# Performance work log

Measured on AMD Instinct MI355X. Metric: run time of the kernel, lower is better.

The kernel has to match this reference:

```python
import jax, jax.numpy as jnp
import numpy as np

N = 50000    # nodes
E = 600000   # edges
D = 128      # emb_dim
L = 5        # num_layer
VA = 64      # atom feature vocab (per column)
VB = 8       # bond feature vocab (per column)
BN_EPS = 1e-5


def setup_inputs() -> dict:
    key = jax.random.key(0)
    ks = jax.random.split(key, 10)
    x = jax.random.randint(ks[0], (N, 9), 0, VA)
    edge_index = jax.random.randint(ks[1], (2, E), 0, N)
    edge_attr = jax.random.randint(ks[2], (E, 3), 0, VB)
    edge_weight = jax.random.uniform(ks[3], (E,), dtype=jnp.float32)
    s = 0.05
    atom_emb = jax.random.normal(ks[4], (9, VA, D), dtype=jnp.float32) * s
    bond_emb = jax.random.normal(ks[5], (L, 3, VB, D), dtype=jnp.float32) * s
    W1 = jax.random.normal(ks[6], (L, D, 2 * D), dtype=jnp.float32) / np.sqrt(D)
    b1 = jnp.zeros((L, 2 * D), jnp.float32)
    bn1_g = jnp.ones((L, 2 * D), jnp.float32)
    bn1_b = jnp.zeros((L, 2 * D), jnp.float32)
    W2 = jax.random.normal(ks[7], (L, 2 * D, D), dtype=jnp.float32) / np.sqrt(2 * D)
    b2 = jnp.zeros((L, D), jnp.float32)
    eps_p = jnp.zeros((L,), jnp.float32)       # GIN eps per layer
    bn_g = jnp.ones((L, D), jnp.float32)       # outer BatchNorm per layer
    bn_b = jnp.zeros((L, D), jnp.float32)
    return dict(x=x, edge_index=edge_index, edge_attr=edge_attr, edge_weight=edge_weight,
                atom_emb=atom_emb, bond_emb=bond_emb, W1=W1, b1=b1, bn1_g=bn1_g,
                bn1_b=bn1_b, W2=W2, b2=b2, eps_p=eps_p, bn_g=bn_g, bn_b=bn_b)


def _bn(z, g, b):
    # training-mode batch norm over the node dimension
    m = z.mean(axis=0)
    v = z.var(axis=0)
    return (z - m) * jax.lax.rsqrt(v + BN_EPS) * g + b


def reference(x, edge_index, edge_attr, edge_weight, atom_emb, bond_emb,
              W1, b1, bn1_g, bn1_b, W2, b2, eps_p, bn_g, bn_b):
    src, dst = edge_index[0], edge_index[1]
    ew = edge_weight[:, None]                                  # [E,1]
    # AtomEncoder: sum of per-column embedding lookups -> [N,D]
    h = sum(atom_emb[f][x[:, f]] for f in range(9))
    for l in range(L):
        # BondEncoder -> [E,D]
        ea = sum(bond_emb[l, f][edge_attr[:, f]] for f in range(3))
        # message: relu(x_j + edge_emb) * edge_weight, scatter-add to dst
        msg = jax.nn.relu(h[src] + ea) * ew                    # [E,D]
        agg = jax.ops.segment_sum(msg, dst, num_segments=N)    # [N,D]
        z = (1.0 + eps_p[l]) * h + agg
        # GIN MLP: Linear -> BN -> ReLU -> Linear
        z = jax.nn.relu(_bn(z @ W1[l] + b1[l], bn1_g[l], bn1_b[l]))
        z = z @ W2[l] + b2[l]
        # outer BatchNorm, ReLU except last layer (dropout is identity at p=0)
        z = _bn(z, bn_g[l], bn_b[l])
        if l < L - 1:
            z = jax.nn.relu(z)
        h = z
    return h  # JK == 'last'
```

## Files before the change

kernel.cpp:

```cpp
#include <hip/hip_runtime.h>

#define NN 50000
#define EE 600000
#define DD 128
#define DD2 256
#define LL 5
#define BN_EPS 1e-5f
#define GXF 512
#define NT1 782
#define SPAD 16

typedef __attribute__((ext_vector_type(8))) _Float16 half8;
typedef __attribute__((ext_vector_type(4))) float f32x4;

__device__ inline unsigned short f2h_bits(float f) {
    _Float16 h = (_Float16)f;
    return __builtin_bit_cast(unsigned short, h);
}
__device__ inline float h2f(unsigned short u) {
    return (float)__builtin_bit_cast(_Float16, u);
}
__device__ inline half8 bnrelu8(half8 v, half8 s, half8 t) {
    half8 r = v * s + t;
#pragma unroll
    for (int k = 0; k < 8; k++) r[k] = (r[k] > (_Float16)0) ? r[k] : (_Float16)0;
    return r;
}


__device__ inline void grid_barrier(int* bar) {
    asm volatile("s_waitcnt vmcnt(0)" ::: "memory");
    __syncthreads();
    if (threadIdx.x == 0) {
        int g = blockIdx.x & 7;
        bool done = false;
        int t = __hip_atomic_fetch_add(&bar[g * 16], 1, __ATOMIC_RELAXED,
                                       __HIP_MEMORY_SCOPE_AGENT);
        if (t == (GXF / 8) - 1) {
            int m = __hip_atomic_fetch_add(&bar[128], 1, __ATOMIC_RELAXED,
                                           __HIP_MEMORY_SCOPE_AGENT);
            if (m == 7) {
                __hip_atomic_store(&bar[144], 1, __ATOMIC_RELAXED, __HIP_MEMORY_SCOPE_AGENT);
                done = true;
            }
        }
        if (!done) {
            while (__hip_atomic_load(&bar[144], __ATOMIC_RELAXED, __HIP_MEMORY_SCOPE_AGENT) == 0)
                __builtin_amdgcn_s_sleep(8);
        }
    }
    __syncthreads();
}


__global__ void hist_kernel(const int* __restrict__ dst, int* __restrict__ counts) {
    int e = blockIdx.x * blockDim.x + threadIdx.x;
    if (e < EE) atomicAdd(&counts[dst[e]], 1);
}

__global__ void scan1_kernel(const int* __restrict__ counts, int* __restrict__ row_ptr,
                             int* __restrict__ blksum) {
    __shared__ int tmp[256];
    int i = blockIdx.x * 256 + threadIdx.x;
    int v = (i < NN) ? counts[i] : 0;
    tmp[threadIdx.x] = v;
    __syncthreads();
    for (int off = 1; off < 256; off <<= 1) {
        int x = 0;
        if (threadIdx.x >= off) x = tmp[threadIdx.x - off];
        __syncthreads();
        if (threadIdx.x >= off) tmp[threadIdx.x] += x;
        __syncthreads();
    }
    if (i < NN) row_ptr[i] = tmp[threadIdx.x] - v;
    if (threadIdx.x == 255) blksum[blockIdx.x] = tmp[255];
}

__global__ void scan2_kernel(int* __restrict__ blksum, int nblocks) {
    __shared__ int tmp[256];
    int v = (threadIdx.x < nblocks) ? blksum[threadIdx.x] : 0;
    tmp[threadIdx.x] = v;
    __syncthreads();
    for (int off = 1; off < 256; off <<= 1) {
        int x = 0;
        if (threadIdx.x >= off) x = tmp[threadIdx.x - off];
        __syncthreads();
        if (threadIdx.x >= off) tmp[threadIdx.x] += x;
        __syncthreads();
    }
    blksum[threadIdx.x] = tmp[threadIdx.x] - v;
}

__global__ void scan3_kernel(int* __restrict__ row_ptr, const int* __restrict__ blksum) {
    int i = blockIdx.x * 256 + threadIdx.x;
    if (i < NN) row_ptr[i] += blksum[blockIdx.x];
    if (i == 0) row_ptr[NN] = EE;
}

__global__ void scatter_kernel(const int* __restrict__ dst, const int* __restrict__ src,
                               const int* __restrict__ edge_attr, const float* __restrict__ ew,
                               const int* __restrict__ row_ptr, int* __restrict__ cursor,
                               uint2* __restrict__ edata) {
    int e = blockIdx.x * blockDim.x + threadIdx.x;
    if (e < EE) {
        int d = dst[e];
        int p = row_ptr[d] + atomicAdd(&cursor[d], 1);
        int cid = edge_attr[3 * e + 0] + 8 * edge_attr[3 * e + 1] + 64 * edge_attr[3 * e + 2];
        uint2 v;
        v.x = (unsigned)src[e];
        v.y = (unsigned)cid | ((unsigned)f2h_bits(ew[e]) << 16);
        edata[p] = v;
    }
}


__global__ void prep_tables_kernel(const float* __restrict__ W1, const float* __restrict__ W2,
                                   const float* __restrict__ bond_emb,
                                   unsigned short* __restrict__ W1t,
                                   unsigned short* __restrict__ W2t,
                                   unsigned short* __restrict__ bsum) {
    const int NW = LL * DD * DD2;
    int idx = blockIdx.x * 256 + threadIdx.x;
    if (idx < NW) {
        int l = idx / (DD * DD2);
        int rem = idx - l * DD * DD2;
        int k = rem / DD2, m = rem - k * DD2;
        W1t[(size_t)l * DD * DD2 + (size_t)m * DD + k] = f2h_bits(W1[idx]);
    } else if (idx < 2 * NW) {
        int j = idx - NW;
        int l = j / (DD * DD2);
        int rem = j - l * DD * DD2;
        int k = rem / DD, m = rem - k * DD;
        W2t[(size_t)l * DD * DD2 + (size_t)m * DD2 + k] = f2h_bits(W2[j]);
    } else if (idx < 2 * NW + LL * 512 * DD) {
        int j = idx - 2 * NW;
        int l = j >> 16;
        int rem = j & 65535;
        int cid = rem >> 7, d = rem & 127;
        int a0 = cid & 7, a1 = (cid >> 3) & 7, a2 = cid >> 6;
        const float* base = bond_emb + (size_t)l * 3 * 8 * DD;
        bsum[j] = f2h_bits(base[a0 * DD + d] + base[(8 + a1) * DD + d] + base[(16 + a2) * DD + d]);
    }
}


__global__ void init_h_kernel(const int* __restrict__ x, const float* __restrict__ atom_emb,
                              unsigned short* __restrict__ h) {
    int n = blockIdx.x * 8 + (threadIdx.x >> 5);
    int lane = threadIdx.x & 31;
    float a0 = 0.f, a1 = 0.f, a2 = 0.f, a3 = 0.f;
#pragma unroll
    for (int f = 0; f < 9; f++) {
        int idx = x[n * 9 + f];
        const float4 v = *(const float4*)(atom_emb + ((size_t)(f * 64 + idx) * DD) + lane * 4);
        a0 += v.x; a1 += v.y; a2 += v.z; a3 += v.w;
    }
    ushort4 o;
    o.x = f2h_bits(a0); o.y = f2h_bits(a1); o.z = f2h_bits(a2); o.w = f2h_bits(a3);
    *(ushort4*)(h + (size_t)n * DD + lane * 4) = o;
}


template <bool FUSE>
__global__ void agg_kernel(const unsigned short* __restrict__ hsrc,
                           const float* __restrict__ stats, const float* __restrict__ g,
                           const float* __restrict__ bb, const int* __restrict__ row_ptr,
                           const uint2* __restrict__ edata,
                           const unsigned short* __restrict__ bsum_l,
                           const float* __restrict__ eps_ptr, unsigned short* __restrict__ Aout) {
    int n = blockIdx.x * 8 + (threadIdx.x >> 5);
    int lane = threadIdx.x & 31;
    int c0 = lane * 4;

    float bs[4] = {1.f, 1.f, 1.f, 1.f}, bt[4] = {0.f, 0.f, 0.f, 0.f};
    if (FUSE) {
        float4 gg = *(const float4*)(g + c0);
        float4 bv = *(const float4*)(bb + c0);
        float gv[4] = {gg.x, gg.y, gg.z, gg.w};
        float bbv[4] = {bv.x, bv.y, bv.z, bv.w};
#pragma unroll
        for (int k = 0; k < 4; k++) {
            float sm = stats[(size_t)(512 + c0 + k) * SPAD];
            float sq = stats[(size_t)(640 + c0 + k) * SPAD];
            float mean = sm * (1.f / NN);
            float var = sq * (1.f / NN) - mean * mean;
            bs[k] = gv[k] * rsqrtf(var + BN_EPS);
            bt[k] = bbv[k] - mean * bs[k];
        }
    }

    auto accum = [&](uint2 ed, uint2 hz, uint2 bz, float* acc) {
        float w = h2f((unsigned short)(ed.y >> 16));
        unsigned int hw[2] = {hz.x, hz.y}, bw[2] = {bz.x, bz.y};
#pragma unroll
        for (int k = 0; k < 2; k++) {
            float hv0 = h2f((unsigned short)(hw[k] & 0xffff));
            float hv1 = h2f((unsigned short)(hw[k] >> 16));
            if (FUSE) {
                hv0 = fmaxf(hv0 * bs[2 * k] + bt[2 * k], 0.f);
                hv1 = fmaxf(hv1 * bs[2 * k + 1] + bt[2 * k + 1], 0.f);
            }
            float m0 = fmaxf(hv0 + h2f((unsigned short)(bw[k] & 0xffff)), 0.f);
            float m1 = fmaxf(hv1 + h2f((unsigned short)(bw[k] >> 16)), 0.f);
            acc[2 * k] += m0 * w;
            acc[2 * k + 1] += m1 * w;
        }
    };

    int beg = row_ptr[n], end = row_ptr[n + 1];
    float acc[4] = {0.f, 0.f, 0.f, 0.f};
    int i = beg;
    for (; i + 4 <= end; i += 4) {
        uint2 e0 = edata[i], e1 = edata[i + 1], e2 = edata[i + 2], e3 = edata[i + 3];
        uint2 h0 = *(const uint2*)(hsrc + (size_t)e0.x * DD + c0);
        uint2 b0 = *(const uint2*)(bsum_l + (size_t)(e0.y & 0xffff) * DD + c0);
        uint2 h1 = *(const uint2*)(hsrc + (size_t)e1.x * DD + c0);
        uint2 b1 = *(const uint2*)(bsum_l + (size_t)(e1.y & 0xffff) * DD + c0);
        uint2 h2 = *(const uint2*)(hsrc + (size_t)e2.x * DD + c0);
        uint2 b2 = *(const uint2*)(bsum_l + (size_t)(e2.y & 0xffff) * DD + c0);
        uint2 h3 = *(const uint2*)(hsrc + (size_t)e3.x * DD + c0);
        uint2 b3 = *(const uint2*)(bsum_l + (size_t)(e3.y & 0xffff) * DD + c0);
        accum(e0, h0, b0, acc);
        accum(e1, h1, b1, acc);
        accum(e2, h2, b2, acc);
        accum(e3, h3, b3, acc);
    }
    for (; i < end; i++) {
        uint2 e0 = edata[i];
        uint2 h0 = *(const uint2*)(hsrc + (size_t)e0.x * DD + c0);
        uint2 b0 = *(const uint2*)(bsum_l + (size_t)(e0.y & 0xffff) * DD + c0);
        accum(e0, h0, b0, acc);
    }

    float eps1 = 1.f + eps_ptr[0];
    uint2 hz = *(const uint2*)(hsrc + (size_t)n * DD + c0);
    unsigned int hw[2] = {hz.x, hz.y};
    float self[4];
#pragma unroll
    for (int k = 0; k < 2; k++) {
        float hv0 = h2f((unsigned short)(hw[k] & 0xffff));
        float hv1 = h2f((unsigned short)(hw[k] >> 16));
        if (FUSE) {
            hv0 = fmaxf(hv0 * bs[2 * k] + bt[2 * k], 0.f);
            hv1 = fmaxf(hv1 * bs[2 * k + 1] + bt[2 * k + 1], 0.f);
        }
        self[2 * k] = hv0;
        self[2 * k + 1] = hv1;
    }
    ushort4 o;
    o.x = f2h_bits(eps1 * self[0] + acc[0]);
    o.y = f2h_bits(eps1 * self[1] + acc[1]);
    o.z = f2h_bits(eps1 * self[2] + acc[2]);
    o.w = f2h_bits(eps1 * self[3] + acc[3]);
    *(ushort4*)(Aout + (size_t)n * DD + c0) = o;
}


__global__ __launch_bounds__(256, 2) void fused_mlp_kernel(
    const unsigned short* __restrict__ A, const unsigned short* __restrict__ W1,
    const float* __restrict__ b1, const unsigned short* __restrict__ W2,
    const float* __restrict__ b2, const float* __restrict__ g1,
    const float* __restrict__ bb1, unsigned short* __restrict__ z2,
    float* __restrict__ statsL, int* bar) {
    __shared__ __align__(16) char ldsb[65536];
    __shared__ __align__(16) float st_sh[2 * DD2];
    const int lane = threadIdx.x & 63;
    const int wave = threadIdx.x >> 6;
    const int lr = lane & 15;
    const int q = lane >> 4;
    const int swz = (lr & 7) << 4;

    {
        const int wcol = wave * 64;
        half8 wf[4][4];
#pragma unroll
        for (int jm = 0; jm < 4; jm++) {
            const unsigned short* p = W1 + (size_t)(wcol + jm * 16 + lr) * DD + q * 8;
#pragma unroll
            for (int ks = 0; ks < 4; ks++)
                wf[jm][ks] = __builtin_bit_cast(half8, *(const int4*)(p + ks * 32));
        }
        float bi[4][4];
#pragma unroll
        for (int jm = 0; jm < 4; jm++)
#pragma unroll
            for (int r = 0; r < 4; r++) bi[jm][r] = b1[wcol + jm * 16 + q * 4 + r];

        float s1[16], sq1[16];
#pragma unroll
        for (int k = 0; k < 16; k++) { s1[k] = 0.f; sq1[k] = 0.f; }

        for (int s = 0; s < 2; s++) {
            int t = blockIdx.x + s * GXF;
            if (t >= NT1) break;
            int row0 = t * 64;
            const unsigned short* ap0 = A + (size_t)(row0 + lr) * DD + q * 8;
            f32x4 acc[4][4];
#pragma unroll
            for (int jm = 0; jm < 4; jm++)
#pragma unroll
                for (int in = 0; in < 4; in++) acc[jm][in] = (f32x4){0.f, 0.f, 0.f, 0.f};
#pragma unroll
            for (int ks = 0; ks < 4; ks++) {
                half8 rf[4];
#pragma unroll
                for (int in = 0; in < 4; in++)
                    rf[in] = __builtin_bit_cast(
                        half8, *(const int4*)(ap0 + (size_t)(in * 16) * DD + ks * 32));
#pragma unroll
                for (int jm = 0; jm < 4; jm++)
#pragma unroll
                    for (int in = 0; in < 4; in++)
                        acc[jm][in] = __builtin_amdgcn_mfma_f32_16x16x32_f16(
                            wf[jm][ks], rf[in], acc[jm][in], 0, 0, 0);
            }
            char* slot = ldsb + s * 32768;
#pragma unroll
            for (int in = 0; in < 4; in++) {
                int row = in * 16 + lr;
                bool rv = (row0 + row) < NN;
                int rbase = row * 512 + wave * 128;
#pragma unroll
                for (int jm = 0; jm < 4; jm++) {
                    ushort4 o;
#pragma unroll
                    for (int r = 0; r < 4; r++) {
                        float v = acc[jm][in][r] + bi[jm][r];
                        ((unsigned short*)&o)[r] = f2h_bits(v);
                        if (rv) {
                            s1[jm * 4 + r] += v;
                            sq1[jm * 4 + r] += v * v;
                        }
                    }
                    *(ushort4*)(slot + ((rbase + jm * 32 + q * 8) ^ swz)) = o;
                }
            }
        }
#pragma unroll
        for (int k = 0; k < 16; k++) {
            float a = s1[k], b = sq1[k];
#pragma unroll
            for (int m = 1; m < 16; m <<= 1) {
                a += __shfl_xor(a, m);
                b += __shfl_xor(b, m);
            }
            if (lr == 0) {
                int c = wcol + (k >> 2) * 16 + q * 4 + (k & 3);
                unsafeAtomicAdd(&statsL[(size_t)c * SPAD], a);
                unsafeAtomicAdd(&statsL[(size_t)(DD2 + c) * SPAD], b);
            }
        }
    }

    grid_barrier(bar);

    {
        for (int c = threadIdx.x; c < DD2; c += 256) {
            float sv = __hip_atomic_load(&statsL[(size_t)c * SPAD], __ATOMIC_RELAXED,
                                         __HIP_MEMORY_SCOPE_AGENT);
            float qv = __hip_atomic_load(&statsL[(size_t)(DD2 + c) * SPAD], __ATOMIC_RELAXED,
                                         __HIP_MEMORY_SCOPE_AGENT);
            float mean = sv * (1.f / NN);
            float var = qv * (1.f / NN) - mean * mean;
            float sc = g1[c] * rsqrtf(var + BN_EPS);
            st_sh[c] = sc;
            st_sh[DD2 + c] = bb1[c] - mean * sc;
        }
        __syncthreads();

        const int cb2 = wave * 32;
        half8 sa[8], ta[8];
#pragma unroll
        for (int ks = 0; ks < 8; ks++) {
            const float* sp = st_sh + ks * 32 + q * 8;
            float4 sA = *(const float4*)(sp);
            float4 sB = *(const float4*)(sp + 4);
            float4 tA = *(const float4*)(sp + DD2);
            float4 tB = *(const float4*)(sp + DD2 + 4);
            sa[ks] = (half8){(_Float16)sA.x, (_Float16)sA.y, (_Float16)sA.z, (_Float16)sA.w,
                             (_Float16)sB.x, (_Float16)sB.y, (_Float16)sB.z, (_Float16)sB.w};
            ta[ks] = (half8){(_Float16)tA.x, (_Float16)tA.y, (_Float16)tA.z, (_Float16)tA.w,
                             (_Float16)tB.x, (_Float16)tB.y, (_Float16)tB.z, (_Float16)tB.w};
        }
        half8 wf2[2][8];
#pragma unroll
        for (int jm = 0; jm < 2; jm++) {
            const unsigned short* p = W2 + (size_t)(cb2 + jm * 16 + lr) * DD2 + q * 8;
#pragma unroll
            for (int ks = 0; ks < 8; ks++)
                wf2[jm][ks] = __builtin_bit_cast(half8, *(const int4*)(p + ks * 32));
        }
        float bi2[2][4];
#pragma unroll
        for (int jm = 0; jm < 2; jm++)
#pragma unroll
            for (int r = 0; r < 4; r++) bi2[jm][r] = b2[cb2 + jm * 16 + q * 4 + r];

        float s2[8], sq2[8];
#pragma unroll
        for (int k = 0; k < 8; k++) { s2[k] = 0.f; sq2[k] = 0.f; }

        for (int s = 0; s < 2; s++) {
            int t = blockIdx.x + s * GXF;
            if (t >= NT1) break;
            int row0 = t * 64;
            char* slot = ldsb + s * 32768;
            f32x4 acc[2][4];
#pragma unroll
            for (int jm = 0; jm < 2; jm++)
#pragma unroll
                for (int in = 0; in < 4; in++) acc[jm][in] = (f32x4){0.f, 0.f, 0.f, 0.f};
#pragma unroll
            for (int ks = 0; ks < 8; ks++) {
                half8 rf[4];
#pragma unroll
                for (int in = 0; in < 4; in++) {
                    int row = in * 16 + lr;
                    half8 z = *(const half8*)(slot + ((row * 512 + ks * 64 + q * 16) ^ swz));
                    rf[in] = bnrelu8(z, sa[ks], ta[ks]);
                }
#pragma unroll
                for (int jm = 0; jm < 2; jm++)
#pragma unroll
                    for (int in = 0; in < 4; in++)
                        acc[jm][in] = __builtin_amdgcn_mfma_f32_16x16x32_f16(
                            wf2[jm][ks], rf[in], acc[jm][in], 0, 0, 0);
            }
#pragma unroll
            for (int in = 0; in < 4; in++) {
                int row = row0 + in * 16 + lr;
                if (row < NN) {
#pragma unroll
                    for (int jm = 0; jm < 2; jm++) {
                        ushort4 o;
#pragma unroll
                        for (int r = 0; r < 4; r++) {
                            float v = acc[jm][in][r] + bi2[jm][r];
                            ((unsigned short*)&o)[r] = f2h_bits(v);
                            s2[jm * 4 + r] += v;
                            sq2[jm * 4 + r] += v * v;
                        }
                        *(ushort4*)(z2 + (size_t)row * DD + cb2 + jm * 16 + q * 4) = o;
                    }
                }
            }
        }
#pragma unroll
        for (int k = 0; k < 8; k++) {
            float a = s2[k], b = sq2[k];
#pragma unroll
            for (int m = 1; m < 16; m <<= 1) {
                a += __shfl_xor(a, m);
                b += __shfl_xor(b, m);
            }
            if (lr == 0) {
                int c = cb2 + (k >> 2) * 16 + q * 4 + (k & 3);
                unsafeAtomicAdd(&statsL[(size_t)(512 + c) * SPAD], a);
                unsafeAtomicAdd(&statsL[(size_t)(640 + c) * SPAD], b);
            }
        }
    }
}


__global__ void bnapply2_last_kernel(const unsigned short* __restrict__ z,
                                     const float* __restrict__ stats, const float* __restrict__ g,
                                     const float* __restrict__ bb, float* __restrict__ fout) {
    __shared__ float s_sh[DD], t_sh[DD];
    if (threadIdx.x < DD) {
        int c = threadIdx.x;
        float mean = stats[(size_t)(512 + c) * SPAD] * (1.f / NN);
        float var = stats[(size_t)(640 + c) * SPAD] * (1.f / NN) - mean * mean;
        float sc = g[c] * rsqrtf(var + BN_EPS);
        s_sh[c] = sc;
        t_sh[c] = bb[c] - mean * sc;
    }
    __syncthreads();
    int i = (blockIdx.x * 256 + threadIdx.x) * 4;
    int c = i & 127;
    uint2 in = *(const uint2*)(z + i);
    float4 out;
    out.x = h2f((unsigned short)(in.x & 0xffff)) * s_sh[c] + t_sh[c];
    out.y = h2f((unsigned short)(in.x >> 16)) * s_sh[c + 1] + t_sh[c + 1];
    out.z = h2f((unsigned short)(in.y & 0xffff)) * s_sh[c + 2] + t_sh[c + 2];
    out.w = h2f((unsigned short)(in.y >> 16)) * s_sh[c + 3] + t_sh[c + 3];
    *(float4*)(fout + i) = out;
}


extern "C" void kernel_launch(void* const* d_in, const int* in_sizes, int n_in,
                              void* d_out, int out_size, void* d_ws, size_t ws_size,
                              hipStream_t stream) {
    const int* x = (const int*)d_in[0];
    const int* edge_index = (const int*)d_in[1];
    const int* edge_attr = (const int*)d_in[2];
    const float* edge_weight = (const float*)d_in[3];
    const float* atom_emb = (const float*)d_in[4];
    const float* bond_emb = (const float*)d_in[5];
    const float* W1 = (const float*)d_in[6];
    const float* b1 = (const float*)d_in[7];
    const float* bn1_g = (const float*)d_in[8];
    const float* bn1_b = (const float*)d_in[9];
    const float* W2 = (const float*)d_in[10];
    const float* b2 = (const float*)d_in[11];
    const float* eps_p = (const float*)d_in[12];
    const float* bn_g = (const float*)d_in[13];
    const float* bn_b = (const float*)d_in[14];
    const int* srcv = edge_index;
    const int* dstv = edge_index + EE;

    char* p = (char*)d_ws;
    auto alloc = [&](size_t bytes) {
        void* r = (void*)p;
        p += (bytes + 255) & ~(size_t)255;
        return r;
    };
    unsigned short* h = (unsigned short*)alloc((size_t)NN * DD * 2);
    unsigned short* A1h = (unsigned short*)alloc((size_t)(NT1 * 64) * DD * 2);
    unsigned short* z2 = (unsigned short*)alloc((size_t)NN * DD * 2);
    uint2* edata = (uint2*)alloc((size_t)EE * 8);
    int* counts = (int*)alloc((size_t)NN * 4);
    int* row_ptr = (int*)alloc((size_t)(NN + 1) * 4);
    int* blksum = (int*)alloc(256 * 4);
    unsigned short* W1t = (unsigned short*)alloc((size_t)LL * DD * DD2 * 2);
    unsigned short* W2t = (unsigned short*)alloc((size_t)LL * DD * DD2 * 2);
    unsigned short* bsum = (unsigned short*)alloc((size_t)LL * 512 * DD * 2);
    const size_t statsFloats = (size_t)LL * 768 * SPAD;
    const size_t barInts = (size_t)LL * 160;
    float* statsP = (float*)alloc(statsFloats * 4 + barInts * 4);
    int* barBase = (int*)(statsP + statsFloats);

    hipMemsetAsync(counts, 0, (size_t)NN * 4, stream);
    hipMemsetAsync(statsP, 0, statsFloats * 4 + barInts * 4, stream);
    hist_kernel<<<(EE + 255) / 256, 256, 0, stream>>>(dstv, counts);
    int nblk = (NN + 255) / 256;
    scan1_kernel<<<nblk, 256, 0, stream>>>(counts, row_ptr, blksum);
    scan2_kernel<<<1, 256, 0, stream>>>(blksum, nblk);
    scan3_kernel<<<nblk, 256, 0, stream>>>(row_ptr, blksum);
    hipMemsetAsync(counts, 0, (size_t)NN * 4, stream);
    scatter_kernel<<<(EE + 255) / 256, 256, 0, stream>>>(dstv, srcv, edge_attr, edge_weight,
                                                         row_ptr, counts, edata);
    prep_tables_kernel<<<(2 * LL * DD * DD2 + LL * 512 * DD + 255) / 256, 256, 0, stream>>>(
        W1, W2, bond_emb, W1t, W2t, bsum);
    init_h_kernel<<<NN / 8, 256, 0, stream>>>(x, atom_emb, h);

    for (int l = 0; l < LL; l++) {
        float* statsL = statsP + (size_t)l * 768 * SPAD;
        const unsigned short* bsum_l = bsum + (size_t)l * 512 * DD;

        if (l == 0) {
            agg_kernel<false><<<NN / 8, 256, 0, stream>>>(h, nullptr, nullptr, nullptr, row_ptr,
                                                          edata, bsum_l, eps_p + l, A1h);
        } else {
            agg_kernel<true><<<NN / 8, 256, 0, stream>>>(
                z2, statsP + (size_t)(l - 1) * 768 * SPAD, bn_g + (l - 1) * DD,
                bn_b + (l - 1) * DD, row_ptr, edata, bsum_l, eps_p + l, A1h);
        }

        fused_mlp_kernel<<<GXF, 256, 0, stream>>>(
            A1h, W1t + (size_t)l * DD * DD2, b1 + l * DD2, W2t + (size_t)l * DD * DD2,
            b2 + l * DD, bn1_g + l * DD2, bn1_b + l * DD2, z2, statsL, barBase + l * 160);
    }

    bnapply2_last_kernel<<<NN * DD / 1024, 256, 0, stream>>>(
        z2, statsP + (size_t)(LL - 1) * 768 * SPAD, bn_g + (LL - 1) * DD, bn_b + (LL - 1) * DD,
        (float*)d_out);
}
```

Measured before the change: 791.5 us.

## Split fused persistent MLP kernel into two GEMM kernels via global intermediate

Replaces the persistent fused MLP kernel, which used a software grid barrier and kept the first-layer output in LDS, with two separate kernels. The first GEMM now writes a 256-wide fp16 intermediate to global memory and the second reads it back. This removes the spin-wait barrier and the 64KB LDS buffer per block, which may let more blocks run and avoids barrier stalls. The cost is an extra kernel launch per layer and roughly 50MB of extra global traffic per layer.

```diff
diff --git a/kernel.cpp b/kernel.cpp
--- a/kernel.cpp
+++ b/kernel.cpp
@@ -6,7 +6,6 @@
 #define DD2 256
 #define LL 5
 #define BN_EPS 1e-5f
-#define GXF 512
 #define NT1 782
 #define SPAD 16
 
@@ -27,30 +26,6 @@
     return r;
 }
 
-
-__device__ inline void grid_barrier(int* bar) {
-    asm volatile("s_waitcnt vmcnt(0)" ::: "memory");
-    __syncthreads();
-    if (threadIdx.x == 0) {
-        int g = blockIdx.x & 7;
-        bool done = false;
-        int t = __hip_atomic_fetch_add(&bar[g * 16], 1, __ATOMIC_RELAXED,
-                                       __HIP_MEMORY_SCOPE_AGENT);
-        if (t == (GXF / 8) - 1) {
-            int m = __hip_atomic_fetch_add(&bar[128], 1, __ATOMIC_RELAXED,
-                                           __HIP_MEMORY_SCOPE_AGENT);
-            if (m == 7) {
-                __hip_atomic_store(&bar[144], 1, __ATOMIC_RELAXED, __HIP_MEMORY_SCOPE_AGENT);
-                done = true;
-            }
-        }
-        if (!done) {
-            while (__hip_atomic_load(&bar[144], __ATOMIC_RELAXED, __HIP_MEMORY_SCOPE_AGENT) == 0)
-                __builtin_amdgcn_s_sleep(8);
-        }
-    }
-    __syncthreads();
-}
 
 
 __global__ void hist_kernel(const int* __restrict__ dst, int* __restrict__ counts) {
@@ -256,208 +231,198 @@
 }
 
 
-__global__ __launch_bounds__(256, 2) void fused_mlp_kernel(
-    const unsigned short* __restrict__ A, const unsigned short* __restrict__ W1,
-    const float* __restrict__ b1, const unsigned short* __restrict__ W2,
-    const float* __restrict__ b2, const float* __restrict__ g1,
-    const float* __restrict__ bb1, unsigned short* __restrict__ z2,
-    float* __restrict__ statsL, int* bar) {
-    __shared__ __align__(16) char ldsb[65536];
+__global__ __launch_bounds__(256, 2) void gemm1_kernel(const unsigned short* __restrict__ A,
+                                                       const unsigned short* __restrict__ W1,
+                                                       const float* __restrict__ b1,
+                                                       unsigned short* __restrict__ z1,
+                                                       float* __restrict__ statsL) {
+    const int lane = threadIdx.x & 63;
+    const int wave = threadIdx.x >> 6;
+    const int lr = lane & 15;
+    const int q = lane >> 4;
+    const int wcol = wave * 64;
+
+    half8 wf[4][4];
+#pragma unroll
+    for (int jm = 0; jm < 4; jm++) {
+        const unsigned short* p = W1 + (size_t)(wcol + jm * 16 + lr) * DD + q * 8;
+#pragma unroll
+        for (int ks = 0; ks < 4; ks++)
+            wf[jm][ks] = __builtin_bit_cast(half8, *(const int4*)(p + ks * 32));
+    }
+    float bi[4][4];
+#pragma unroll
+    for (int jm = 0; jm < 4; jm++)
+#pragma unroll
+        for (int r = 0; r < 4; r++) bi[jm][r] = b1[wcol + jm * 16 + q * 4 + r];
+
+    int row0 = blockIdx.x * 64;
+    const unsigned short* ap0 = A + (size_t)(row0 + lr) * DD + q * 8;
+    f32x4 acc[4][4];
+#pragma unroll
+    for (int jm = 0; jm < 4; jm++)
+#pragma unroll
+        for (int in = 0; in < 4; in++) acc[jm][in] = (f32x4){0.f, 0.f, 0.f, 0.f};
+#pragma unroll
+    for (int ks = 0; ks < 4; ks++) {
+        half8 rf[4];
+#pragma unroll
+        for (int in = 0; in < 4; in++)
+            rf[in] =
+                __builtin_bit_cast(half8, *(const int4*)(ap0 + (size_t)(in * 16) * DD + ks * 32));
+#pragma unroll
+        for (int jm = 0; jm < 4; jm++)
+#pragma unroll
+            for (int in = 0; in < 4; in++)
+                acc[jm][in] =
+                    __builtin_amdgcn_mfma_f32_16x16x32_f16(wf[jm][ks], rf[in], acc[jm][in], 0, 0, 0);
+    }
+
+    float s1[16], sq1[16];
+#pragma unroll
+    for (int k = 0; k < 16; k++) { s1[k] = 0.f; sq1[k] = 0.f; }
+#pragma unroll
+    for (int in = 0; in < 4; in++) {
+        int row = row0 + in * 16 + lr;
+        bool rv = row < NN;
+#pragma unroll
+        for (int jm = 0; jm < 4; jm++) {
+            ushort4 o;
+#pragma unroll
+            for (int r = 0; r < 4; r++) {
+                float v = acc[jm][in][r] + bi[jm][r];
+                ((unsigned short*)&o)[r] = f2h_bits(v);
+                if (rv) {
+                    s1[jm * 4 + r] += v;
+                    sq1[jm * 4 + r] += v * v;
+                }
+            }
+            if (rv) *(ushort4*)(z1 + (size_t)row * DD2 + wcol + jm * 16 + q * 4) = o;
+        }
+    }
+#pragma unroll
+    for (int k = 0; k < 16; k++) {
+        float a = s1[k], b = sq1[k];
+#pragma unroll
+        for (int m = 1; m < 16; m <<= 1) {
+            a += __shfl_xor(a, m);
+            b += __shfl_xor(b, m);
+        }
+        if (lr == 0) {
+            int c = wcol + (k >> 2) * 16 + q * 4 + (k & 3);
+            unsafeAtomicAdd(&statsL[(size_t)c * SPAD], a);
+            unsafeAtomicAdd(&statsL[(size_t)(DD2 + c) * SPAD], b);
+        }
+    }
+}
+
+
+__global__ __launch_bounds__(256, 2) void gemm2_kernel(
+    const unsigned short* __restrict__ z1, const unsigned short* __restrict__ W2,
+    const float* __restrict__ b2, const float* __restrict__ g1, const float* __restrict__ bb1,
+    unsigned short* __restrict__ z2, float* __restrict__ statsL) {
     __shared__ __align__(16) float st_sh[2 * DD2];
     const int lane = threadIdx.x & 63;
     const int wave = threadIdx.x >> 6;
     const int lr = lane & 15;
     const int q = lane >> 4;
-    const int swz = (lr & 7) << 4;
 
     {
-        const int wcol = wave * 64;
-        half8 wf[4][4];
-#pragma unroll
-        for (int jm = 0; jm < 4; jm++) {
-            const unsigned short* p = W1 + (size_t)(wcol + jm * 16 + lr) * DD + q * 8;
-#pragma unroll
-            for (int ks = 0; ks < 4; ks++)
-                wf[jm][ks] = __builtin_bit_cast(half8, *(const int4*)(p + ks * 32));
-        }
-        float bi[4][4];
-#pragma unroll
-        for (int jm = 0; jm < 4; jm++)
-#pragma unroll
-            for (int r = 0; r < 4; r++) bi[jm][r] = b1[wcol + jm * 16 + q * 4 + r];
-
-        float s1[16], sq1[16];
-#pragma unroll
-        for (int k = 0; k < 16; k++) { s1[k] = 0.f; sq1[k] = 0.f; }
-
-        for (int s = 0; s < 2; s++) {
-            int t = blockIdx.x + s * GXF;
-            if (t >= NT1) break;
-            int row0 = t * 64;
-            const unsigned short* ap0 = A + (size_t)(row0 + lr) * DD + q * 8;
-            f32x4 acc[4][4];
-#pragma unroll
-            for (int jm = 0; jm < 4; jm++)
-#pragma unroll
-                for (int in = 0; in < 4; in++) acc[jm][in] = (f32x4){0.f, 0.f, 0.f, 0.f};
-#pragma unroll
-            for (int ks = 0; ks < 4; ks++) {
-                half8 rf[4];
-#pragma unroll
-                for (int in = 0; in < 4; in++)
-                    rf[in] = __builtin_bit_cast(
-                        half8, *(const int4*)(ap0 + (size_t)(in * 16) * DD + ks * 32));
-#pragma unroll
-                for (int jm = 0; jm < 4; jm++)
-#pragma unroll
-                    for (int in = 0; in < 4; in++)
-                        acc[jm][in] = __builtin_amdgcn_mfma_f32_16x16x32_f16(
-                            wf[jm][ks], rf[in], acc[jm][in], 0, 0, 0);
+        int c = threadIdx.x;
+        float sv = statsL[(size_t)c * SPAD];
+        float qv = statsL[(size_t)(DD2 + c) * SPAD];
+        float mean = sv * (1.f / NN);
+        float var = qv * (1.f / NN) - mean * mean;
+        float sc = g1[c] * rsqrtf(var + BN_EPS);
+        st_sh[c] = sc;
+        st_sh[DD2 + c] = bb1[c] - mean * sc;
+    }
+    __syncthreads();
+
+    const int cb2 = wave * 32;
+    half8 sa[8], ta[8];
+#pragma unroll
+    for (int ks = 0; ks < 8; ks++) {
+        const float* sp = st_sh + ks * 32 + q * 8;
+        float4 sA = *(const float4*)(sp);
+        float4 sB = *(const float4*)(sp + 4);
+        float4 tA = *(const float4*)(sp + DD2);
+        float4 tB = *(const float4*)(sp + DD2 + 4);
+        sa[ks] = (half8){(_Float16)sA.x, (_Float16)sA.y, (_Float16)sA.z, (_Float16)sA.w,
+                         (_Float16)sB.x, (_Float16)sB.y, (_Float16)sB.z, (_Float16)sB.w};
+        ta[ks] = (half8){(_Float16)tA.x, (_Float16)tA.y, (_Float16)tA.z, (_Float16)tA.w,
+                         (_Float16)tB.x, (_Float16)tB.y, (_Float16)tB.z, (_Float16)tB.w};
+    }
+    half8 wf2[2][8];
+#pragma unroll
+    for (int jm = 0; jm < 2; jm++) {
+        const unsigned short* p = W2 + (size_t)(cb2 + jm * 16 + lr) * DD2 + q * 8;
+#pragma unroll
+        for (int ks = 0; ks < 8; ks++)
+            wf2[jm][ks] = __builtin_bit_cast(half8, *(const int4*)(p + ks * 32));
+    }
+    float bi2[2][4];
+#pragma unroll
+    for (int jm = 0; jm < 2; jm++)
+#pragma unroll
+        for (int r = 0; r < 4; r++) bi2[jm][r] = b2[cb2 + jm * 16 + q * 4 + r];
+
+    int row0 = blockIdx.x * 64;
+    f32x4 acc[2][4];
+#pragma unroll
+    for (int jm = 0; jm < 2; jm++)
+#pragma unroll
+        for (int in = 0; in < 4; in++) acc[jm][in] = (f32x4){0.f, 0.f, 0.f, 0.f};
+#pragma unroll
+    for (int ks = 0; ks < 8; ks++) {
+        half8 rf[4];
+#pragma unroll
+        for (int in = 0; in < 4; in++) {
+            int row = row0 + in * 16 + lr;
+            half8 z = *(const half8*)(z1 + (size_t)row * DD2 + ks * 32 + q * 8);
+            rf[in] = bnrelu8(z, sa[ks], ta[ks]);
+        }
+#pragma unroll
+        for (int jm = 0; jm < 2; jm++)
+#pragma unroll
+            for (int in = 0; in < 4; in++)
+                acc[jm][in] = __builtin_amdgcn_mfma_f32_16x16x32_f16(wf2[jm][ks], rf[in],
+                                                                     acc[jm][in], 0, 0, 0);
+    }
+
+    float s2[8], sq2[8];
+#pragma unroll
+    for (int k = 0; k < 8; k++) { s2[k] = 0.f; sq2[k] = 0.f; }
+#pragma unroll
+    for (int in = 0; in < 4; in++) {
+        int row = row0 + in * 16 + lr;
+        if (row < NN) {
+#pragma unroll
+            for (int jm = 0; jm < 2; jm++) {
+                ushort4 o;
+#pragma unroll
+                for (int r = 0; r < 4; r++) {
+                    float v = acc[jm][in][r] + bi2[jm][r];
+                    ((unsigned short*)&o)[r] = f2h_bits(v);
+                    s2[jm * 4 + r] += v;
+                    sq2[jm * 4 + r] += v * v;
+                }
+                *(ushort4*)(z2 + (size_t)row * DD + cb2 + jm * 16 + q * 4) = o;
             }
-            char* slot = ldsb + s * 32768;
-#pragma unroll
-            for (int in = 0; in < 4; in++) {
-                int row = in * 16 + lr;
-                bool rv = (row0 + row) < NN;
-                int rbase = row * 512 + wave * 128;
-#pragma unroll
-                for (int jm = 0; jm < 4; jm++) {
-                    ushort4 o;
-#pragma unroll
-                    for (int r = 0; r < 4; r++) {
-                        float v = acc[jm][in][r] + bi[jm][r];
-                        ((unsigned short*)&o)[r] = f2h_bits(v);
-                        if (rv) {
-                            s1[jm * 4 + r] += v;
-                            sq1[jm * 4 + r] += v * v;
-                        }
-                    }
-                    *(ushort4*)(slot + ((rbase + jm * 32 + q * 8) ^ swz)) = o;
-                }
-            }
-        }
-#pragma unroll
-        for (int k = 0; k < 16; k++) {
-            float a = s1[k], b = sq1[k];
-#pragma unroll
-            for (int m = 1; m < 16; m <<= 1) {
-                a += __shfl_xor(a, m);
-                b += __shfl_xor(b, m);
-            }
-            if (lr == 0) {
-                int c = wcol + (k >> 2) * 16 + q * 4 + (k & 3);
-                unsafeAtomicAdd(&statsL[(size_t)c * SPAD], a);
-                unsafeAtomicAdd(&statsL[(size_t)(DD2 + c) * SPAD], b);
-            }
-        }
-    }
-
-    grid_barrier(bar);
-
-    {
-        for (int c = threadIdx.x; c < DD2; c += 256) {
-            float sv = __hip_atomic_load(&statsL[(size_t)c * SPAD], __ATOMIC_RELAXED,
-                                         __HIP_MEMORY_SCOPE_AGENT);
-            float qv = __hip_atomic_load(&statsL[(size_t)(DD2 + c) * SPAD], __ATOMIC_RELAXED,
-                                         __HIP_MEMORY_SCOPE_AGENT);
-            float mean = sv * (1.f / NN);
-            float var = qv * (1.f / NN) - mean * mean;
-            float sc = g1[c] * rsqrtf(var + BN_EPS);
-            st_sh[c] = sc;
-            st_sh[DD2 + c] = bb1[c] - mean * sc;
-        }
-        __syncthreads();
-
-        const int cb2 = wave * 32;
-        half8 sa[8], ta[8];
-#pragma unroll
-        for (int ks = 0; ks < 8; ks++) {
-            const float* sp = st_sh + ks * 32 + q * 8;
-            float4 sA = *(const float4*)(sp);
-            float4 sB = *(const float4*)(sp + 4);
-            float4 tA = *(const float4*)(sp + DD2);
-            float4 tB = *(const float4*)(sp + DD2 + 4);
-            sa[ks] = (half8){(_Float16)sA.x, (_Float16)sA.y, (_Float16)sA.z, (_Float16)sA.w,
-                             (_Float16)sB.x, (_Float16)sB.y, (_Float16)sB.z, (_Float16)sB.w};
-            ta[ks] = (half8){(_Float16)tA.x, (_Float16)tA.y, (_Float16)tA.z, (_Float16)tA.w,
-                             (_Float16)tB.x, (_Float16)tB.y, (_Float16)tB.z, (_Float16)tB.w};
-        }
-        half8 wf2[2][8];
-#pragma unroll
-        for (int jm = 0; jm < 2; jm++) {
-            const unsigned short* p = W2 + (size_t)(cb2 + jm * 16 + lr) * DD2 + q * 8;
-#pragma unroll
-            for (int ks = 0; ks < 8; ks++)
-                wf2[jm][ks] = __builtin_bit_cast(half8, *(const int4*)(p + ks * 32));
-        }
-        float bi2[2][4];
-#pragma unroll
-        for (int jm = 0; jm < 2; jm++)
-#pragma unroll
-            for (int r = 0; r < 4; r++) bi2[jm][r] = b2[cb2 + jm * 16 + q * 4 + r];
-
-        float s2[8], sq2[8];
-#pragma unroll
-        for (int k = 0; k < 8; k++) { s2[k] = 0.f; sq2[k] = 0.f; }
-
-        for (int s = 0; s < 2; s++) {
-            int t = blockIdx.x + s * GXF;
-            if (t >= NT1) break;
-            int row0 = t * 64;
-            char* slot = ldsb + s * 32768;
-            f32x4 acc[2][4];
-#pragma unroll
-            for (int jm = 0; jm < 2; jm++)
-#pragma unroll
-                for (int in = 0; in < 4; in++) acc[jm][in] = (f32x4){0.f, 0.f, 0.f, 0.f};
-#pragma unroll
-            for (int ks = 0; ks < 8; ks++) {
-                half8 rf[4];
-#pragma unroll
-                for (int in = 0; in < 4; in++) {
-                    int row = in * 16 + lr;
-                    half8 z = *(const half8*)(slot + ((row * 512 + ks * 64 + q * 16) ^ swz));
-                    rf[in] = bnrelu8(z, sa[ks], ta[ks]);
-                }
-#pragma unroll
-                for (int jm = 0; jm < 2; jm++)
-#pragma unroll
-                    for (int in = 0; in < 4; in++)
-                        acc[jm][in] = __builtin_amdgcn_mfma_f32_16x16x32_f16(
-                            wf2[jm][ks], rf[in], acc[jm][in], 0, 0, 0);
-            }
-#pragma unroll
-            for (int in = 0; in < 4; in++) {
-                int row = row0 + in * 16 + lr;
-                if (row < NN) {
-#pragma unroll
-                    for (int jm = 0; jm < 2; jm++) {
-                        ushort4 o;
-#pragma unroll
-                        for (int r = 0; r < 4; r++) {
-                            float v = acc[jm][in][r] + bi2[jm][r];
-                            ((unsigned short*)&o)[r] = f2h_bits(v);
-                            s2[jm * 4 + r] += v;
-                            sq2[jm * 4 + r] += v * v;
-                        }
-                        *(ushort4*)(z2 + (size_t)row * DD + cb2 + jm * 16 + q * 4) = o;
-                    }
-                }
-            }
-        }
-#pragma unroll
-        for (int k = 0; k < 8; k++) {
-            float a = s2[k], b = sq2[k];
-#pragma unroll
-            for (int m = 1; m < 16; m <<= 1) {
-                a += __shfl_xor(a, m);
-                b += __shfl_xor(b, m);
-            }
-            if (lr == 0) {
-                int c = cb2 + (k >> 2) * 16 + q * 4 + (k & 3);
-                unsafeAtomicAdd(&statsL[(size_t)(512 + c) * SPAD], a);
-                unsafeAtomicAdd(&statsL[(size_t)(640 + c) * SPAD], b);
-            }
+        }
+    }
+#pragma unroll
+    for (int k = 0; k < 8; k++) {
+        float a = s2[k], b = sq2[k];
+#pragma unroll
+        for (int m = 1; m < 16; m <<= 1) {
+            a += __shfl_xor(a, m);
+            b += __shfl_xor(b, m);
+        }
+        if (lr == 0) {
+            int c = cb2 + (k >> 2) * 16 + q * 4 + (k & 3);
+            unsafeAtomicAdd(&statsL[(size_t)(512 + c) * SPAD], a);
+            unsafeAtomicAdd(&statsL[(size_t)(640 + c) * SPAD], b);
         }
     }
 }
@@ -517,6 +482,7 @@
     };
     unsigned short* h = (unsigned short*)alloc((size_t)NN * DD * 2);
     unsigned short* A1h = (unsigned short*)alloc((size_t)(NT1 * 64) * DD * 2);
+    unsigned short* z1 = (unsigned short*)alloc((size_t)(NT1 * 64) * DD2 * 2);
     unsigned short* z2 = (unsigned short*)alloc((size_t)NN * DD * 2);
     uint2* edata = (uint2*)alloc((size_t)EE * 8);
     int* counts = (int*)alloc((size_t)NN * 4);
@@ -526,12 +492,10 @@
     unsigned short* W2t = (unsigned short*)alloc((size_t)LL * DD * DD2 * 2);
     unsigned short* bsum = (unsigned short*)alloc((size_t)LL * 512 * DD * 2);
     const size_t statsFloats = (size_t)LL * 768 * SPAD;
-    const size_t barInts = (size_t)LL * 160;
-    float* statsP = (float*)alloc(statsFloats * 4 + barInts * 4);
-    int* barBase = (int*)(statsP + statsFloats);
+    float* statsP = (float*)alloc(statsFloats * 4);
 
     hipMemsetAsync(counts, 0, (size_t)NN * 4, stream);
-    hipMemsetAsync(statsP, 0, statsFloats * 4 + barInts * 4, stream);
+    hipMemsetAsync(statsP, 0, statsFloats * 4, stream);
     hist_kernel<<<(EE + 255) / 256, 256, 0, stream>>>(dstv, counts);
     int nblk = (NN + 255) / 256;
     scan1_kernel<<<nblk, 256, 0, stream>>>(counts, row_ptr, blksum);
@@ -557,9 +521,10 @@
                 bn_b + (l - 1) * DD, row_ptr, edata, bsum_l, eps_p + l, A1h);
         }
 
-        fused_mlp_kernel<<<GXF, 256, 0, stream>>>(
-            A1h, W1t + (size_t)l * DD * DD2, b1 + l * DD2, W2t + (size_t)l * DD * DD2,
-            b2 + l * DD, bn1_g + l * DD2, bn1_b + l * DD2, z2, statsL, barBase + l * 160);
+        gemm1_kernel<<<NT1, 256, 0, stream>>>(A1h, W1t + (size_t)l * DD * DD2, b1 + l * DD2, z1,
+                                              statsL);
+        gemm2_kernel<<<NT1, 256, 0, stream>>>(z1, W2t + (size_t)l * DD * DD2, b2 + l * DD,
+                                              bn1_g + l * DD2, bn1_b + l * DD2, z2, statsL);
     }
 
     bnapply2_last_kernel<<<NN * DD / 1024, 256, 0, stream>>>(
```

Result: slower. 973.3 us (+23.0%).
